# Performance work log

Hardware: AMD Instinct MI355X
Metric: run time of the kernel (lower is better)

## Reference

```python
import jax, jax.numpy as jnp
import numpy as np

NUM_NODES = 1_000_000
IN_F, HID_F, OUT_F = 128, 128, 128
N0, N1, T = 16384, 4096, 16


def _safediv(a, b):
    return a / jnp.where(b == 0, jnp.ones_like(b), b)


def _conv(h, nodeset, nb_nodes, nb_w, Qw, Qb, Ww, Wb):
    # gather self + neighbor embeddings (irregular access)
    h_self = h[nodeset]                                   # [n, in]
    h_nb = h[nb_nodes]                                    # [n, T, in]
    q = jax.nn.leaky_relu(jnp.einsum('nti,hi->nth', h_nb, Qw) + Qb)
    agg = _safediv((nb_w[:, :, None] * q).sum(1), nb_w.sum(1, keepdims=True))  # [n, hid]
    h_cat = jnp.concatenate([h_self, agg], axis=1)        # [n, in+hid]
    h_new = jax.nn.leaky_relu(h_cat @ Ww.T + Wb)          # [n, out]
    nrm = jnp.linalg.norm(h_new, axis=1, keepdims=True)
    return _safediv(h_new, nrm)


def setup_inputs() -> dict:
    key = jax.random.key(0)
    ks = jax.random.split(key, 16)
    xav = lambda k, o, i: jax.random.uniform(k, (o, i), jnp.float32, -1.0, 1.0) * jnp.sqrt(6.0 / (o + i)) * jnp.sqrt(2.0)
    return {
        'h': jax.random.normal(ks[0], (NUM_NODES, IN_F), jnp.float32),
        'Qw0': xav(ks[1], HID_F, IN_F), 'Qb0': jnp.zeros((HID_F,), jnp.float32),
        'Ww0': xav(ks[2], HID_F, IN_F + HID_F), 'Wb0': jnp.zeros((HID_F,), jnp.float32),
        'Qw1': xav(ks[3], OUT_F, HID_F), 'Qb1': jnp.zeros((OUT_F,), jnp.float32),
        'Ww1': xav(ks[4], OUT_F, HID_F + OUT_F), 'Wb1': jnp.zeros((OUT_F,), jnp.float32),
        'nodeset0': jax.random.randint(ks[5], (N0,), 0, NUM_NODES, jnp.int32),
        'nb_nodes0': jax.random.randint(ks[6], (N0, T), 0, NUM_NODES, jnp.int32),
        'nb_weights0': jax.random.uniform(ks[7], (N0, T), jnp.float32),
        'nodeset1': jax.random.randint(ks[8], (N1,), 0, NUM_NODES, jnp.int32),
        'nb_nodes1': jax.random.randint(ks[9], (N1, T), 0, NUM_NODES, jnp.int32),
        'nb_weights1': jax.random.uniform(ks[10], (N1, T), jnp.float32),
    }


def reference(h, Qw0, Qb0, Ww0, Wb0, Qw1, Qb1, Ww1, Wb1,
              nodeset0, nb_nodes0, nb_weights0,
              nodeset1, nb_nodes1, nb_weights1):
    # layer 0: conv then scatter back into embedding table
    new0 = _conv(h, nodeset0, nb_nodes0, nb_weights0, Qw0, Qb0, Ww0, Wb0)
    h = h.at[nodeset0].set(new0)
    # layer 1
    new1 = _conv(h, nodeset1, nb_nodes1, nb_weights1, Qw1, Qb1, Ww1, Wb1)
    h = h.at[nodeset1].set(new1)
    return h[nodeset1]  # [N1, OUT_F]
```

## Files before the change

### kernel.cpp

```cpp
#include <hip/hip_runtime.h>
#include <hip/hip_bf16.h>
#include <math.h>

#define NN 1000000
#define F 128
#define N0 16384
#define N1 4096

typedef __attribute__((ext_vector_type(8))) short bf16x8;
typedef __attribute__((ext_vector_type(4))) float f32x4;

__device__ inline unsigned short f2b(float f) {
    union { float f; unsigned u; } v; v.f = f;
    unsigned r = v.u + 0x7FFFu + ((v.u >> 16) & 1u);
    return (unsigned short)(r >> 16);
}

__device__ inline bf16x8 pack8(float4 a, float4 b) {
    union { __hip_bfloat162 h2[4]; bf16x8 v; } u;
    u.h2[0] = __float22bfloat162_rn(make_float2(a.x, a.y));
    u.h2[1] = __float22bfloat162_rn(make_float2(a.z, a.w));
    u.h2[2] = __float22bfloat162_rn(make_float2(b.x, b.y));
    u.h2[3] = __float22bfloat162_rn(make_float2(b.z, b.w));
    return u.v;
}


__global__ void k_prep(const int* __restrict__ ns0, const int* __restrict__ ns1,
                       int* __restrict__ map0, int* __restrict__ map1,
                       const float* __restrict__ Qw0, const float* __restrict__ Qw1,
                       const float* __restrict__ Ww0, const float* __restrict__ Ww1,
                       unsigned short* __restrict__ Qw0b, unsigned short* __restrict__ Qw1b,
                       unsigned short* __restrict__ Ww0b, unsigned short* __restrict__ Ww1b) {
    int i = blockIdx.x * blockDim.x + threadIdx.x;
    int nt = gridDim.x * blockDim.x;
    if (i < N0) atomicMax(&map0[ns0[i]], i);
    if (i < N1) atomicMax(&map1[ns1[i]], i);
    for (int j = i; j < 128 * 128; j += nt) { Qw0b[j] = f2b(Qw0[j]); Qw1b[j] = f2b(Qw1[j]); }
    for (int j = i; j < 128 * 256; j += nt) { Ww0b[j] = f2b(Ww0[j]); Ww1b[j] = f2b(Ww1[j]); }
}


__global__ __launch_bounds__(256) void k_qagg(
    const float* __restrict__ h, const float* __restrict__ newprev,
    const int* __restrict__ mapprev,
    const int* __restrict__ nb, const float* __restrict__ nbw,
    const unsigned short* __restrict__ Qwb, const float* __restrict__ Qb,
    unsigned short* __restrict__ aggb)
{
    __shared__ unsigned short lQ[128 * 128];
    const int tid = threadIdx.x;
    const int wid = tid >> 6, lane = tid & 63;
    const int row = lane & 15, kg = lane >> 4;
    const long nodebase = (long)blockIdx.x * 8 + wid * 2;

    float4 av[2][8];
#pragma unroll
    for (int nn = 0; nn < 2; ++nn) {
        long node = nodebase + nn;
        int g = nb[node * 16 + row];
        const float* src = h + (size_t)g * F;
        if (mapprev) {
            int p = mapprev[g];
            if (p >= 0) src = newprev + (size_t)p * F;
        }
        const float4* s4 = (const float4*)src;
#pragma unroll
        for (int kk = 0; kk < 4; ++kk) {
            av[nn][kk * 2]     = s4[kk * 8 + kg * 2];
            av[nn][kk * 2 + 1] = s4[kk * 8 + kg * 2 + 1];
        }
    }

    for (int c = tid; c < 2048; c += 256) {
        int j = c >> 4;
        uint4 v = ((const uint4*)Qwb)[c];
        *(uint4*)((char*)lQ + ((c << 4) ^ ((j & 7) << 4))) = v;
    }
    __syncthreads();

    bf16x8 A[2][4];
#pragma unroll
    for (int nn = 0; nn < 2; ++nn)
#pragma unroll
        for (int kk = 0; kk < 4; ++kk)
            A[nn][kk] = pack8(av[nn][kk * 2], av[nn][kk * 2 + 1]);

    f32x4 acc[2][8];
#pragma unroll
    for (int nn = 0; nn < 2; ++nn)
#pragma unroll
        for (int jt = 0; jt < 8; ++jt)
            acc[nn][jt] = (f32x4){0.f, 0.f, 0.f, 0.f};

#pragma unroll
    for (int kk = 0; kk < 4; ++kk) {
        bf16x8 Bf[8];
#pragma unroll
        for (int jt = 0; jt < 8; ++jt) {
            int j = jt * 16 + row;
            int byte = ((j << 8) + (kk << 6) + (kg << 4)) ^ ((j & 7) << 4);
            Bf[jt] = *(bf16x8*)((char*)lQ + byte);
        }
#pragma unroll
        for (int jt = 0; jt < 8; ++jt) {
            acc[0][jt] = __builtin_amdgcn_mfma_f32_16x16x32_bf16(A[0][kk], Bf[jt], acc[0][jt], 0, 0, 0);
            acc[1][jt] = __builtin_amdgcn_mfma_f32_16x16x32_bf16(A[1][kk], Bf[jt], acc[1][jt], 0, 0, 0);
        }
    }

#pragma unroll
    for (int nn = 0; nn < 2; ++nn) {
        long node = nodebase + nn;
        float w[4];
#pragma unroll
        for (int r = 0; r < 4; ++r) w[r] = nbw[node * 16 + kg * 4 + r];
        float ws = w[0] + w[1] + w[2] + w[3];
        ws += __shfl_xor(ws, 16);
        ws += __shfl_xor(ws, 32);
        float inv = (ws == 0.f) ? 1.f : 1.f / ws;
#pragma unroll
        for (int jt = 0; jt < 8; ++jt) {
            float qb = Qb[jt * 16 + row];
            float t = 0.f;
#pragma unroll
            for (int r = 0; r < 4; ++r) {
                float v = acc[nn][jt][r] + qb;
                v = v > 0.f ? v : 0.01f * v;
                t = fmaf(w[r], v, t);
            }
            t += __shfl_xor(t, 16);
            t += __shfl_xor(t, 32);
            if (lane < 16) aggb[node * 128 + jt * 16 + lane] = f2b(t * inv);
        }
    }
}


__global__ __launch_bounds__(256) void k_dense(
    const float* __restrict__ h, const float* __restrict__ newprev,
    const int* __restrict__ mapprev,
    const int* __restrict__ nodeset, const unsigned short* __restrict__ aggb,
    const unsigned short* __restrict__ Wwb, const float* __restrict__ Wb,
    float* __restrict__ outnew)
{
    __shared__ unsigned short lW[128 * 256];
    const int tid = threadIdx.x;
    const int wid = tid >> 6, lane = tid & 63;
    const int row = lane & 15, kg = lane >> 4;
    const long mbase = (long)blockIdx.x * 64 + wid * 16;
    const long m = mbase + row;

    int gs = nodeset[m];
    const float* src = h + (size_t)gs * F;
    if (mapprev) {
        int p = mapprev[gs];
        if (p >= 0) src = newprev + (size_t)p * F;
    }
    float4 av[8];
    const float4* s4 = (const float4*)src;
#pragma unroll
    for (int kk = 0; kk < 4; ++kk) {
        av[kk * 2]     = s4[kk * 8 + kg * 2];
        av[kk * 2 + 1] = s4[kk * 8 + kg * 2 + 1];
    }
    bf16x8 Aagg[4];
    const bf16x8* a4 = (const bf16x8*)(aggb + m * 128);
#pragma unroll
    for (int kk = 0; kk < 4; ++kk) Aagg[kk] = a4[kk * 4 + kg];

    for (int c = tid; c < 4096; c += 256) {
        int j = c >> 5;
        uint4 v = ((const uint4*)Wwb)[c];
        *(uint4*)((char*)lW + ((c << 4) ^ ((j & 7) << 4))) = v;
    }
    __syncthreads();

    bf16x8 A[8];
#pragma unroll
    for (int kk = 0; kk < 4; ++kk) {
        A[kk] = pack8(av[kk * 2], av[kk * 2 + 1]);
        A[4 + kk] = Aagg[kk];
    }

    f32x4 acc[8];
#pragma unroll
    for (int jt = 0; jt < 8; ++jt) acc[jt] = (f32x4){0.f, 0.f, 0.f, 0.f};

#pragma unroll
    for (int kk = 0; kk < 8; ++kk) {
        bf16x8 Bf[8];
#pragma unroll
        for (int jt = 0; jt < 8; ++jt) {
            int j = jt * 16 + row;
            int byte = ((j << 9) + (kk << 6) + (kg << 4)) ^ ((j & 7) << 4);
            Bf[jt] = *(bf16x8*)((char*)lW + byte);
        }
#pragma unroll
        for (int jt = 0; jt < 8; ++jt)
            acc[jt] = __builtin_amdgcn_mfma_f32_16x16x32_bf16(A[kk], Bf[jt], acc[jt], 0, 0, 0);
    }

    float ss[4] = {0.f, 0.f, 0.f, 0.f};
#pragma unroll
    for (int jt = 0; jt < 8; ++jt) {
        float wb = Wb[jt * 16 + row];
#pragma unroll
        for (int r = 0; r < 4; ++r) {
            float v = acc[jt][r] + wb;
            v = v > 0.f ? v : 0.01f * v;
            acc[jt][r] = v;
            ss[r] = fmaf(v, v, ss[r]);
        }
    }
#pragma unroll
    for (int r = 0; r < 4; ++r) {
        ss[r] += __shfl_xor(ss[r], 1);
        ss[r] += __shfl_xor(ss[r], 2);
        ss[r] += __shfl_xor(ss[r], 4);
        ss[r] += __shfl_xor(ss[r], 8);
    }
    float invn[4];
#pragma unroll
    for (int r = 0; r < 4; ++r) {
        float n = sqrtf(ss[r]);
        invn[r] = (n == 0.f) ? 1.f : 1.f / n;
    }
#pragma unroll
    for (int jt = 0; jt < 8; ++jt)
#pragma unroll
        for (int r = 0; r < 4; ++r)
            outnew[(size_t)(mbase + kg * 4 + r) * F + jt * 16 + row] = acc[jt][r] * invn[r];
}


__global__ void k_fix(const int* __restrict__ map1, const int* __restrict__ ns1,
                      float* __restrict__ out, int n) {
    int i = blockIdx.x * blockDim.x + threadIdx.x;
    if (i < n) {
        int p = map1[ns1[i]];
        if (p != i) {
            float4* o = (float4*)out;
#pragma unroll
            for (int c = 0; c < 32; ++c) o[(size_t)i * 32 + c] = o[(size_t)p * 32 + c];
        }
    }
}


extern "C" void kernel_launch(void* const* d_in, const int* in_sizes, int n_in,
                              void* d_out, int out_size, void* d_ws, size_t ws_size,
                              hipStream_t stream) {
    const float* h    = (const float*)d_in[0];
    const float* Qw0  = (const float*)d_in[1];
    const float* Qb0  = (const float*)d_in[2];
    const float* Ww0  = (const float*)d_in[3];
    const float* Wb0  = (const float*)d_in[4];
    const float* Qw1  = (const float*)d_in[5];
    const float* Qb1  = (const float*)d_in[6];
    const float* Ww1  = (const float*)d_in[7];
    const float* Wb1  = (const float*)d_in[8];
    const int*   ns0  = (const int*)d_in[9];
    const int*   nb0  = (const int*)d_in[10];
    const float* nbw0 = (const float*)d_in[11];
    const int*   ns1  = (const int*)d_in[12];
    const int*   nb1  = (const int*)d_in[13];
    const float* nbw1 = (const float*)d_in[14];

    int* map0 = (int*)d_ws;
    int* map1 = map0 + NN;
    float* new0 = (float*)(map1 + NN);
    unsigned short* aggb = (unsigned short*)(new0 + (size_t)N0 * F);
    unsigned short* Qw0b = aggb + (size_t)N0 * F;
    unsigned short* Qw1b = Qw0b + 128 * 128;
    unsigned short* Ww0b = Qw1b + 128 * 128;
    unsigned short* Ww1b = Ww0b + 128 * 256;

    hipMemsetAsync(map0, 0xFF, (size_t)2 * NN * sizeof(int), stream);
    k_prep<<<64, 256, 0, stream>>>(ns0, ns1, map0, map1,
                                   Qw0, Qw1, Ww0, Ww1, Qw0b, Qw1b, Ww0b, Ww1b);

    k_qagg<<<N0 / 8, 256, 0, stream>>>(h, nullptr, nullptr, nb0, nbw0, Qw0b, Qb0, aggb);
    k_dense<<<N0 / 64, 256, 0, stream>>>(h, nullptr, nullptr, ns0, aggb, Ww0b, Wb0, new0);

    k_qagg<<<N1 / 8, 256, 0, stream>>>(h, new0, map0, nb1, nbw1, Qw1b, Qb1, aggb);
    k_dense<<<N1 / 64, 256, 0, stream>>>(h, new0, map0, ns1, aggb, Ww1b, Wb1, (float*)d_out);

    k_fix<<<(N1 + 255) / 256, 256, 0, stream>>>(map1, ns1, (float*)d_out, N1);
}
```

Before: 95.08 us.

## Fuse neighbor aggregation and dense projection into one per-layer kernel

Merges the q-aggregation and dense kernels into a single 512-thread kernel per layer. Each block handles 16 nodes and stages the self embeddings plus the aggregated features in shared memory. The dense GEMM reads weights straight from global memory, with each wave owning 16 output columns and a cross-wave shared-memory reduction for the L2 norm. The layer-0 output is now stored as bf16, which halves intermediate traffic and removes the aggb round trip and two launches. The cost is fewer blocks and an extra sync, plus somewhat lower precision for the layer-0 result that feeds layer 1.

Result: faster. 91.44 us (-3.8%).

```diff
diff --git a/kernel.cpp b/kernel.cpp
--- a/kernel.cpp
+++ b/kernel.cpp
@@ -41,50 +41,92 @@
 }
 
 
-__global__ __launch_bounds__(256) void k_qagg(
-    const float* __restrict__ h, const float* __restrict__ newprev,
+__global__ __launch_bounds__(512) void k_layer(
+    const float* __restrict__ h, const unsigned short* __restrict__ newprevb,
     const int* __restrict__ mapprev,
-    const int* __restrict__ nb, const float* __restrict__ nbw,
+    const int* __restrict__ nodeset, const int* __restrict__ nb,
+    const float* __restrict__ nbw,
     const unsigned short* __restrict__ Qwb, const float* __restrict__ Qb,
-    unsigned short* __restrict__ aggb)
+    const unsigned short* __restrict__ Wwb, const float* __restrict__ Wb,
+    float* __restrict__ outf, unsigned short* __restrict__ outb)
 {
     __shared__ unsigned short lQ[128 * 128];
+    __shared__ unsigned short lA[16 * 256];
+    __shared__ float sred[8][16];
     const int tid = threadIdx.x;
     const int wid = tid >> 6, lane = tid & 63;
     const int row = lane & 15, kg = lane >> 4;
-    const long nodebase = (long)blockIdx.x * 8 + wid * 2;
-
+    const long mbase = (long)blockIdx.x * 16;
+
+    float4 sv[4];
+    uint4 sb[2];
+    bool sredir = false;
+    const int sq = tid & 7;
+    if (tid < 128) {
+        int sr = tid >> 3;
+        int gs = nodeset[mbase + sr];
+        int p = mapprev ? mapprev[gs] : -1;
+        if (p >= 0) {
+            sredir = true;
+            const uint4* s = (const uint4*)(newprevb + (size_t)p * F + sq * 16);
+            sb[0] = s[0]; sb[1] = s[1];
+        } else {
+            const float4* s = (const float4*)(h + (size_t)gs * F + sq * 16);
+            sv[0] = s[0]; sv[1] = s[1]; sv[2] = s[2]; sv[3] = s[3];
+        }
+    }
+
+    const long nodebase = mbase + wid * 2;
     float4 av[2][8];
+    bf16x8 Ab[2][4];
+    bool redir[2];
 #pragma unroll
     for (int nn = 0; nn < 2; ++nn) {
         long node = nodebase + nn;
         int g = nb[node * 16 + row];
-        const float* src = h + (size_t)g * F;
-        if (mapprev) {
-            int p = mapprev[g];
-            if (p >= 0) src = newprev + (size_t)p * F;
-        }
-        const float4* s4 = (const float4*)src;
-#pragma unroll
-        for (int kk = 0; kk < 4; ++kk) {
-            av[nn][kk * 2]     = s4[kk * 8 + kg * 2];
-            av[nn][kk * 2 + 1] = s4[kk * 8 + kg * 2 + 1];
-        }
-    }
-
-    for (int c = tid; c < 2048; c += 256) {
+        int p = mapprev ? mapprev[g] : -1;
+        redir[nn] = (p >= 0);
+        if (p >= 0) {
+            const bf16x8* s = (const bf16x8*)(newprevb + (size_t)p * F);
+#pragma unroll
+            for (int kk = 0; kk < 4; ++kk) Ab[nn][kk] = s[kk * 4 + kg];
+        } else {
+            const float4* s4 = (const float4*)(h + (size_t)g * F);
+#pragma unroll
+            for (int kk = 0; kk < 4; ++kk) {
+                av[nn][kk * 2]     = s4[kk * 8 + kg * 2];
+                av[nn][kk * 2 + 1] = s4[kk * 8 + kg * 2 + 1];
+            }
+        }
+    }
+
+    for (int c = tid; c < 2048; c += 512) {
         int j = c >> 4;
         uint4 v = ((const uint4*)Qwb)[c];
         *(uint4*)((char*)lQ + ((c << 4) ^ ((j & 7) << 4))) = v;
     }
+
+    if (tid < 128) {
+        int sr = tid >> 3;
+        int b0 = sr * 512 + sq * 32;
+        int swz = (sr & 7) << 4;
+        if (sredir) {
+            *(uint4*)((char*)lA + (b0 ^ swz)) = sb[0];
+            *(uint4*)((char*)lA + ((b0 + 16) ^ swz)) = sb[1];
+        } else {
+            *(bf16x8*)((char*)lA + (b0 ^ swz)) = pack8(sv[0], sv[1]);
+            *(bf16x8*)((char*)lA + ((b0 + 16) ^ swz)) = pack8(sv[2], sv[3]);
+        }
+    }
+
+#pragma unroll
+    for (int nn = 0; nn < 2; ++nn)
+        if (!redir[nn]) {
+#pragma unroll
+            for (int kk = 0; kk < 4; ++kk)
+                Ab[nn][kk] = pack8(av[nn][kk * 2], av[nn][kk * 2 + 1]);
+        }
     __syncthreads();
-
-    bf16x8 A[2][4];
-#pragma unroll
-    for (int nn = 0; nn < 2; ++nn)
-#pragma unroll
-        for (int kk = 0; kk < 4; ++kk)
-            A[nn][kk] = pack8(av[nn][kk * 2], av[nn][kk * 2 + 1]);
 
     f32x4 acc[2][8];
 #pragma unroll
@@ -104,14 +146,15 @@
         }
 #pragma unroll
         for (int jt = 0; jt < 8; ++jt) {
-            acc[0][jt] = __builtin_amdgcn_mfma_f32_16x16x32_bf16(A[0][kk], Bf[jt], acc[0][jt], 0, 0, 0);
-            acc[1][jt] = __builtin_amdgcn_mfma_f32_16x16x32_bf16(A[1][kk], Bf[jt], acc[1][jt], 0, 0, 0);
+            acc[0][jt] = __builtin_amdgcn_mfma_f32_16x16x32_bf16(Ab[0][kk], Bf[jt], acc[0][jt], 0, 0, 0);
+            acc[1][jt] = __builtin_amdgcn_mfma_f32_16x16x32_bf16(Ab[1][kk], Bf[jt], acc[1][jt], 0, 0, 0);
         }
     }
 
 #pragma unroll
     for (int nn = 0; nn < 2; ++nn) {
         long node = nodebase + nn;
+        int nl = wid * 2 + nn;
         float w[4];
 #pragma unroll
         for (int r = 0; r < 4; ++r) w[r] = nbw[node * 16 + kg * 4 + r];
@@ -131,87 +174,31 @@
             }
             t += __shfl_xor(t, 16);
             t += __shfl_xor(t, 32);
-            if (lane < 16) aggb[node * 128 + jt * 16 + lane] = f2b(t * inv);
-        }
-    }
-}
-
-
-__global__ __launch_bounds__(256) void k_dense(
-    const float* __restrict__ h, const float* __restrict__ newprev,
-    const int* __restrict__ mapprev,
-    const int* __restrict__ nodeset, const unsigned short* __restrict__ aggb,
-    const unsigned short* __restrict__ Wwb, const float* __restrict__ Wb,
-    float* __restrict__ outnew)
-{
-    __shared__ unsigned short lW[128 * 256];
-    const int tid = threadIdx.x;
-    const int wid = tid >> 6, lane = tid & 63;
-    const int row = lane & 15, kg = lane >> 4;
-    const long mbase = (long)blockIdx.x * 64 + wid * 16;
-    const long m = mbase + row;
-
-    int gs = nodeset[m];
-    const float* src = h + (size_t)gs * F;
-    if (mapprev) {
-        int p = mapprev[gs];
-        if (p >= 0) src = newprev + (size_t)p * F;
-    }
-    float4 av[8];
-    const float4* s4 = (const float4*)src;
-#pragma unroll
-    for (int kk = 0; kk < 4; ++kk) {
-        av[kk * 2]     = s4[kk * 8 + kg * 2];
-        av[kk * 2 + 1] = s4[kk * 8 + kg * 2 + 1];
-    }
-    bf16x8 Aagg[4];
-    const bf16x8* a4 = (const bf16x8*)(aggb + m * 128);
-#pragma unroll
-    for (int kk = 0; kk < 4; ++kk) Aagg[kk] = a4[kk * 4 + kg];
-
-    for (int c = tid; c < 4096; c += 256) {
-        int j = c >> 5;
-        uint4 v = ((const uint4*)Wwb)[c];
-        *(uint4*)((char*)lW + ((c << 4) ^ ((j & 7) << 4))) = v;
+            if (lane < 16) {
+                int byte = (nl * 512 + 256 + jt * 32 + lane * 2) ^ ((nl & 7) << 4);
+                *(unsigned short*)((char*)lA + byte) = f2b(t * inv);
+            }
+        }
     }
     __syncthreads();
 
-    bf16x8 A[8];
-#pragma unroll
-    for (int kk = 0; kk < 4; ++kk) {
-        A[kk] = pack8(av[kk * 2], av[kk * 2 + 1]);
-        A[4 + kk] = Aagg[kk];
-    }
-
-    f32x4 acc[8];
-#pragma unroll
-    for (int jt = 0; jt < 8; ++jt) acc[jt] = (f32x4){0.f, 0.f, 0.f, 0.f};
-
+    const int j = wid * 16 + row;
+    f32x4 dacc = (f32x4){0.f, 0.f, 0.f, 0.f};
 #pragma unroll
     for (int kk = 0; kk < 8; ++kk) {
-        bf16x8 Bf[8];
-#pragma unroll
-        for (int jt = 0; jt < 8; ++jt) {
-            int j = jt * 16 + row;
-            int byte = ((j << 9) + (kk << 6) + (kg << 4)) ^ ((j & 7) << 4);
-            Bf[jt] = *(bf16x8*)((char*)lW + byte);
-        }
-#pragma unroll
-        for (int jt = 0; jt < 8; ++jt)
-            acc[jt] = __builtin_amdgcn_mfma_f32_16x16x32_bf16(A[kk], Bf[jt], acc[jt], 0, 0, 0);
-    }
-
-    float ss[4] = {0.f, 0.f, 0.f, 0.f};
-#pragma unroll
-    for (int jt = 0; jt < 8; ++jt) {
-        float wb = Wb[jt * 16 + row];
-#pragma unroll
-        for (int r = 0; r < 4; ++r) {
-            float v = acc[jt][r] + wb;
-            v = v > 0.f ? v : 0.01f * v;
-            acc[jt][r] = v;
-            ss[r] = fmaf(v, v, ss[r]);
-        }
+        bf16x8 a = *(bf16x8*)((char*)lA + ((row * 512 + kk * 64 + kg * 16) ^ ((row & 7) << 4)));
+        bf16x8 b = ((const bf16x8*)(Wwb + (size_t)j * 256))[kk * 4 + kg];
+        dacc = __builtin_amdgcn_mfma_f32_16x16x32_bf16(a, b, dacc, 0, 0, 0);
+    }
+
+    float wb = Wb[j];
+    float ss[4];
+#pragma unroll
+    for (int r = 0; r < 4; ++r) {
+        float v = dacc[r] + wb;
+        v = v > 0.f ? v : 0.01f * v;
+        dacc[r] = v;
+        ss[r] = v * v;
     }
 #pragma unroll
     for (int r = 0; r < 4; ++r) {
@@ -220,17 +207,29 @@
         ss[r] += __shfl_xor(ss[r], 4);
         ss[r] += __shfl_xor(ss[r], 8);
     }
+    if (row == 0) {
+#pragma unroll
+        for (int r = 0; r < 4; ++r) sred[wid][kg * 4 + r] = ss[r];
+    }
+    __syncthreads();
     float invn[4];
 #pragma unroll
     for (int r = 0; r < 4; ++r) {
-        float n = sqrtf(ss[r]);
+        float s = 0.f;
+#pragma unroll
+        for (int w8 = 0; w8 < 8; ++w8) s += sred[w8][kg * 4 + r];
+        float n = sqrtf(s);
         invn[r] = (n == 0.f) ? 1.f : 1.f / n;
     }
-#pragma unroll
-    for (int jt = 0; jt < 8; ++jt)
+    if (outf) {
 #pragma unroll
         for (int r = 0; r < 4; ++r)
-            outnew[(size_t)(mbase + kg * 4 + r) * F + jt * 16 + row] = acc[jt][r] * invn[r];
+            outf[(size_t)(mbase + kg * 4 + r) * F + j] = dacc[r] * invn[r];
+    } else {
+#pragma unroll
+        for (int r = 0; r < 4; ++r)
+            outb[(size_t)(mbase + kg * 4 + r) * F + j] = f2b(dacc[r] * invn[r]);
+    }
 }
 
 
@@ -269,9 +268,8 @@
 
     int* map0 = (int*)d_ws;
     int* map1 = map0 + NN;
-    float* new0 = (float*)(map1 + NN);
-    unsigned short* aggb = (unsigned short*)(new0 + (size_t)N0 * F);
-    unsigned short* Qw0b = aggb + (size_t)N0 * F;
+    unsigned short* new0b = (unsigned short*)(map1 + NN);
+    unsigned short* Qw0b = new0b + (size_t)N0 * F;
     unsigned short* Qw1b = Qw0b + 128 * 128;
     unsigned short* Ww0b = Qw1b + 128 * 128;
     unsigned short* Ww1b = Ww0b + 128 * 256;
@@ -280,11 +278,11 @@
     k_prep<<<64, 256, 0, stream>>>(ns0, ns1, map0, map1,
                                    Qw0, Qw1, Ww0, Ww1, Qw0b, Qw1b, Ww0b, Ww1b);
 
-    k_qagg<<<N0 / 8, 256, 0, stream>>>(h, nullptr, nullptr, nb0, nbw0, Qw0b, Qb0, aggb);
-    k_dense<<<N0 / 64, 256, 0, stream>>>(h, nullptr, nullptr, ns0, aggb, Ww0b, Wb0, new0);
-
-    k_qagg<<<N1 / 8, 256, 0, stream>>>(h, new0, map0, nb1, nbw1, Qw1b, Qb1, aggb);
-    k_dense<<<N1 / 64, 256, 0, stream>>>(h, new0, map0, ns1, aggb, Ww1b, Wb1, (float*)d_out);
+    k_layer<<<N0 / 16, 512, 0, stream>>>(h, nullptr, nullptr, ns0, nb0, nbw0,
+                                         Qw0b, Qb0, Ww0b, Wb0, nullptr, new0b);
+
+    k_layer<<<N1 / 16, 512, 0, stream>>>(h, new0b, map0, ns1, nb1, nbw1,
+                                         Qw1b, Qb1, Ww1b, Wb1, (float*)d_out, nullptr);
 
     k_fix<<<(N1 + 255) / 256, 256, 0, stream>>>(map1, ns1, (float*)d_out, N1);
 }
```
